# Performance work log

Measured on AMD Instinct MI355X. Metric: run time of the kernel, lower is better.

Reference implementation:

```python
import jax, jax.numpy as jnp
import numpy as np

C = 512
C8 = C // 8
B, H, W = 4, 64, 64


def _conv1x1(x, w, b):
    # x: (B, Cin, H, W), w: (Cout, Cin), b: (Cout,)
    return jnp.einsum('oi,bihw->bohw', w, x) + b[None, :, None, None]


def setup_inputs() -> dict:
    key = jax.random.key(0)
    ks = jax.random.split(key, 16)
    s = 0.02
    inp = {
        'x': jax.random.normal(ks[0], (B, C, H, W), dtype=jnp.float32),
        'wpq': jax.random.normal(ks[1], (C8, C), dtype=jnp.float32) * s,
        'bpq': jnp.zeros((C8,), jnp.float32),
        'wpk': jax.random.normal(ks[2], (C8, C), dtype=jnp.float32) * s,
        'bpk': jnp.zeros((C8,), jnp.float32),
        'wpv': jax.random.normal(ks[3], (C, C), dtype=jnp.float32) * s,
        'bpv': jnp.zeros((C,), jnp.float32),
        'wcq': jax.random.normal(ks[4], (C, C), dtype=jnp.float32) * s,
        'bcq': jnp.zeros((C,), jnp.float32),
        'wck': jax.random.normal(ks[5], (C, C), dtype=jnp.float32) * s,
        'bck': jnp.zeros((C,), jnp.float32),
        'wcv': jax.random.normal(ks[6], (C, C), dtype=jnp.float32) * s,
        'bcv': jnp.zeros((C,), jnp.float32),
        # gammas are zero-init in torch; use small nonzero values so both
        # attention branches contribute to the output numerically.
        'gpos': jax.random.normal(ks[7], (1,), dtype=jnp.float32) * 0.1,
        'gchan': jax.random.normal(ks[8], (1,), dtype=jnp.float32) * 0.1,
    }
    return inp


def reference(x, wpq, bpq, wpk, bpk, wpv, bpv, wcq, bcq, wck, bck, wcv, bcv, gpos, gchan):
    b, c, h, w = x.shape
    n = h * w
    # ---- position attention ----
    pos_q = _conv1x1(x, wpq, bpq).reshape(b, C8, n)           # (b, C/8, N)
    pos_k = _conv1x1(x, wpk, bpk).reshape(b, C8, n)           # (b, C/8, N)
    pos_v = _conv1x1(x, wpv, bpv).reshape(b, c, n)            # (b, C, N)
    pos_attn = jax.nn.softmax(jnp.einsum('bcq,bck->bqk', pos_q, pos_k), axis=-1)  # (b, N, N)
    pos_out = jnp.einsum('bck,bqk->bcq', pos_v, pos_attn).reshape(b, c, h, w)
    pos_out = gpos * pos_out + x
    # ---- channel attention ----
    chan_q = _conv1x1(pos_out, wcq, bcq).reshape(b, c, n)
    chan_k = _conv1x1(pos_out, wck, bck).reshape(b, c, n)
    chan_v = _conv1x1(pos_out, wcv, bcv).reshape(b, c, n)
    chan_attn = jax.nn.softmax(jnp.einsum('bin,bjn->bij', chan_q, chan_k), axis=-1)  # (b, C, C)
    chan_out = jnp.einsum('bij,bjn->bin', chan_attn, chan_v).reshape(b, c, h, w)
    return gchan * chan_out + pos_out
```

## Files before the change

kernel.cpp:

```cpp
#include <hip/hip_runtime.h>
#include <hip/hip_bf16.h>
#include <math.h>

typedef __bf16 bf16;
typedef __attribute__((ext_vector_type(8))) __bf16 bf16x8;
typedef __attribute__((ext_vector_type(4))) __bf16 bf16x4;
typedef __attribute__((ext_vector_type(4))) float f32x4;

#define DEVI static __device__ __forceinline__

DEVI int swzb(int row, int ch) { return ((ch ^ (row & 7)) << 4); }

DEVI void gl_lds16(const void* g, void* l) {
  __builtin_amdgcn_global_load_lds(
      (const __attribute__((address_space(1))) unsigned int*)g,
      (__attribute__((address_space(3))) unsigned int*)l, 16, 0, 0);
}

template<int N> DEVI void wait_vm() {
  if constexpr (N == 0) asm volatile("s_waitcnt vmcnt(0)" ::: "memory");
  else if constexpr (N == 4) asm volatile("s_waitcnt vmcnt(4)" ::: "memory");
  else if constexpr (N == 6) asm volatile("s_waitcnt vmcnt(6)" ::: "memory");
  else if constexpr (N == 8) asm volatile("s_waitcnt vmcnt(8)" ::: "memory");
}
DEVI void sbar() {
  __builtin_amdgcn_sched_barrier(0);
  __builtin_amdgcn_s_barrier();
  __builtin_amdgcn_sched_barrier(0);
}

__global__ __launch_bounds__(256) void prep_weights(
    const float* __restrict__ wpq, const float* __restrict__ wpk,
    const float* __restrict__ wpv, const float* __restrict__ wcq,
    const float* __restrict__ wck, const float* __restrict__ wcv,
    const float* __restrict__ bpq, const float* __restrict__ bpk,
    bf16* __restrict__ wqk, bf16* __restrict__ wpvb, bf16* __restrict__ wcqb,
    bf16* __restrict__ wckb, bf16* __restrict__ wcvT, float* __restrict__ bqk)
{
  int i = blockIdx.x * 256 + threadIdx.x;
  switch (blockIdx.y) {
    case 0: if (i < 64*512)  wqk[i]          = (bf16)wpq[i]; break;
    case 1: if (i < 64*512)  wqk[64*512 + i] = (bf16)wpk[i]; break;
    case 2: if (i < 512*512) wpvb[i] = (bf16)wpv[i]; break;
    case 3: if (i < 512*512) wcqb[i] = (bf16)wcq[i]; break;
    case 4: if (i < 512*512) wckb[i] = (bf16)wck[i]; break;
    case 5: if (i < 512*512) { int t = i >> 9, j = i & 511; wcvT[i] = (bf16)wcv[j*512 + t]; } break;
    case 6: if (i < 64) bqk[i] = bpq[i]; else if (i < 128) bqk[i] = bpk[i - 64]; break;
  }
}

__global__ __launch_bounds__(256) void transpose_x(const float* __restrict__ x, bf16* __restrict__ xbT)
{
  __shared__ float t[32][33];
  int b = blockIdx.z, n0 = blockIdx.x * 32, c0 = blockIdx.y * 32;
  int tx = threadIdx.x & 31, ty = threadIdx.x >> 5;
#pragma unroll
  for (int i = 0; i < 4; ++i)
    t[ty + 8*i][tx] = x[((size_t)b*512 + c0 + ty + 8*i)*4096 + n0 + tx];
  __syncthreads();
#pragma unroll
  for (int i = 0; i < 4; ++i)
    xbT[((size_t)b*4096 + n0 + ty + 8*i)*512 + c0 + tx] = (bf16)t[tx][ty + 8*i];
}

struct GemmP {
  const bf16* A; const bf16* Bt; void* C;
  long aS, bS;
  long cSbytes;
  int lda, ldb, ldc, K;
  const float* biasM; const float* biasN;
  const float* e_bq; const float* e_v; const float* e_u; const float* e_bk; float e_nn;
  long vS, uS;
  const float* gchan; const float* Abv; const bf16* Pres; long abvS, presS;
};

template<int BM, int BN, int BIAS, int EPI>
__global__ __launch_bounds__(256) void gemm_k(GemmP p)
{
  constexpr int QF = BM / 32;
  constexpr int CF = BN / 32;
  constexpr int NBUF = (BM + BN <= 192) ? 3 : 2;
  constexpr int LOADS = (BM + BN) / 32;
  __shared__ __align__(16) char sa[NBUF][BM * 128];
  __shared__ __align__(16) char sb[NBUF][BN * 128];
  const int tid = threadIdx.x, lane = tid & 63, w = tid >> 6;
  const int g = lane >> 4, l15 = lane & 15;
  const int bm = blockIdx.x * BM, bn = blockIdx.y * BN, bz = blockIdx.z;
  const bf16* A  = p.A  + (size_t)bz * p.aS;
  const bf16* Bt = p.Bt + (size_t)bz * p.bS;
  char* Cb = (char*)p.C + (size_t)bz * p.cSbytes;
  const int wm = (w & 1) * (BM / 2), wn = (w >> 1) * (BN / 2);
  const int srow = tid >> 3, sch = tid & 7;

  f32x4 acc[QF][CF];
#pragma unroll
  for (int i = 0; i < QF; ++i)
#pragma unroll
    for (int j = 0; j < CF; ++j) acc[i][j] = f32x4{0.f, 0.f, 0.f, 0.f};

  auto stage = [&](int k0, int bi) {
#pragma unroll
    for (int it = 0; it < BM / 32; ++it) {
      int r = it * 32 + srow;
      gl_lds16(A + (size_t)(bm + r) * p.lda + k0 + ((sch ^ (r & 7)) * 8),
               sa[bi] + (it * 32 + w * 8) * 128);
    }
#pragma unroll
    for (int it = 0; it < BN / 32; ++it) {
      int r = it * 32 + srow;
      gl_lds16(Bt + (size_t)(bn + r) * p.ldb + k0 + ((sch ^ (r & 7)) * 8),
               sb[bi] + (it * 32 + w * 8) * 128);
    }
  };
  auto compute = [&](int bi) {
#pragma unroll
    for (int kc = 0; kc < 2; ++kc) {
      bf16x8 af[QF], bfr[CF];
#pragma unroll
      for (int qf = 0; qf < QF; ++qf) {
        int row = wm + 16 * qf + l15;
        af[qf] = *(const bf16x8*)(sa[bi] + row * 128 + swzb(row, g + 4 * kc));
      }
#pragma unroll
      for (int cf = 0; cf < CF; ++cf) {
        int row = wn + 16 * cf + l15;
        bfr[cf] = *(const bf16x8*)(sb[bi] + row * 128 + swzb(row, g + 4 * kc));
      }
      __builtin_amdgcn_s_setprio(1);
#pragma unroll
      for (int qf = 0; qf < QF; ++qf)
#pragma unroll
        for (int cf = 0; cf < CF; ++cf)
          acc[qf][cf] = __builtin_amdgcn_mfma_f32_16x16x32_bf16(af[qf], bfr[cf], acc[qf][cf], 0, 0, 0);
      __builtin_amdgcn_s_setprio(0);
    }
  };

  const int nk = p.K >> 6;
  if constexpr (NBUF == 3) {
    stage(0, 0);
    if (nk > 1) { stage(64, 1); wait_vm<LOADS>(); } else wait_vm<0>();
    sbar();
    int bi = 0;
    for (int t = 0; t < nk; ++t) {
      int b2 = bi + 2; if (b2 >= 3) b2 -= 3;
      if (t + 2 < nk) stage((t + 2) << 6, b2);
      compute(bi);
      if (t + 1 < nk) {
        if (t + 2 < nk) wait_vm<LOADS>(); else wait_vm<0>();
        sbar();
      }
      if (++bi == 3) bi = 0;
    }
  } else {
    stage(0, 0);
    __syncthreads();
    for (int t = 0; t < nk; ++t) {
      const int cur = t & 1;
      if (t + 1 < nk) stage((t + 1) << 6, cur ^ 1);
      compute(cur);
      __syncthreads();
    }
  }

  float gc = 0.f;
  const float* AbvB = nullptr; const bf16* PresB = nullptr;
  const float* eV = nullptr; const float* eU = nullptr;
  if (EPI == 3) { gc = p.gchan[0]; AbvB = p.Abv + (size_t)bz * p.abvS; PresB = p.Pres + (size_t)bz * p.presS; }
  if (EPI == 2) { eV = p.e_v + (size_t)bz * p.vS; eU = p.e_u + (size_t)bz * p.uS; }

#pragma unroll
  for (int qf = 0; qf < QF; ++qf)
#pragma unroll
    for (int cf = 0; cf < CF; ++cf)
#pragma unroll
      for (int r = 0; r < 4; ++r) {
        int m = bm + wm + 16 * qf + 4 * g + r;
        int n = bn + wn + 16 * cf + l15;
        float v = acc[qf][cf][r];
        if (BIAS == 1) v += p.biasM[m];
        if (BIAS == 2) v += p.biasN[n];
        size_t idx = (size_t)m * p.ldc + n;
        if (EPI == 0) ((bf16*)Cb)[idx] = (bf16)v;
        else if (EPI == 1) ((float*)Cb)[idx] = v;
        else if (EPI == 2) {
          v += p.e_bq[m] * eV[n] + eU[m] * p.e_bk[n] + p.e_nn * p.e_bq[m] * p.e_bk[n];
          ((float*)Cb)[idx] = v;
        } else {
          v = gc * (v + AbvB[m]) + (float)PresB[idx];
          ((float*)Cb)[idx] = v;
        }
      }
}

__global__ __launch_bounds__(512, 4) void flash_pos(
    const bf16* __restrict__ QKT, const bf16* __restrict__ Vv,
    const float* __restrict__ x, const float* __restrict__ gpos,
    bf16* __restrict__ Pb, bf16* __restrict__ PTb)
{
  extern __shared__ char sm[];
  char* Vlds = sm + 16384;
  char* Plds = sm + 49152;
  float* Och  = (float*)sm;
  float* lsum = (float*)(sm + 57344);

  const int tid = threadIdx.x, lane = tid & 63, w = tid >> 6;
  const int g = lane >> 4, l15 = lane & 15;
  const int wq = w & 3;
  const int wh = w >> 2;
  const int phys = blockIdx.x;
  const int b  = (phys & 7) >> 1;
  const int ch = phys & 1;
  const int q0 = (phys >> 3) << 6;
  const int c0 = ch << 8;

  const bf16* QKTb = QKT + (size_t)b * 4096 * 128;
  const bf16* Vb   = Vv  + (size_t)b * 512 * 4096;

  const bf16* qrow = QKTb + (size_t)(q0 + 16 * wq + l15) * 128;
  bf16x8 qa0 = *(const bf16x8*)(qrow + 8 * g);
  bf16x8 qa1 = *(const bf16x8*)(qrow + 32 + 8 * g);

  f32x4 acc[4][2];
#pragma unroll
  for (int i = 0; i < 4; ++i) { acc[i][0] = f32x4{0.f,0.f,0.f,0.f}; acc[i][1] = f32x4{0.f,0.f,0.f,0.f}; }
  f32x4 l_r = f32x4{0.f, 0.f, 0.f, 0.f};

  const int srow = tid >> 3, sch = tid & 7;
  const bf16* Ksrc = QKTb + (size_t)srow * 128 + 64 + ((sch ^ (srow & 7)) * 8);

  gl_lds16(Ksrc, sm + w * 1024);
#pragma unroll
  for (int it = 0; it < 4; ++it) {
    int r = it * 64 + srow;
    gl_lds16(Vb + (size_t)(c0 + r) * 4096 + ((sch ^ (r & 7)) * 8),
             Vlds + (it * 64 + w * 8) * 128);
  }
  asm volatile("s_waitcnt vmcnt(0)" ::: "memory");
  sbar();

  for (int t = 0; t < 64; ++t) {
    const char* Kcur = sm + ((t & 1) << 13);
    char* Knext = sm + (((t + 1) & 1) << 13);
    const int ktn = (t + 1) & 63;
    gl_lds16(Ksrc + (size_t)ktn * 8192, Knext + w * 1024);
    __builtin_amdgcn_sched_barrier(0);
    f32x4 s0 = f32x4{0.f,0.f,0.f,0.f}, s1 = f32x4{0.f,0.f,0.f,0.f};
    {
      const int r0 = 32 * wh + l15, r1 = r0 + 16;
      bf16x8 k00 = *(const bf16x8*)(Kcur + r0 * 128 + swzb(r0, g));
      bf16x8 k01 = *(const bf16x8*)(Kcur + r0 * 128 + swzb(r0, g + 4));
      bf16x8 k10 = *(const bf16x8*)(Kcur + r1 * 128 + swzb(r1, g));
      bf16x8 k11 = *(const bf16x8*)(Kcur + r1 * 128 + swzb(r1, g + 4));
      __builtin_amdgcn_s_setprio(1);
      s0 = __builtin_amdgcn_mfma_f32_16x16x32_bf16(qa0, k00, s0, 0, 0, 0);
      s0 = __builtin_amdgcn_mfma_f32_16x16x32_bf16(qa1, k01, s0, 0, 0, 0);
      s1 = __builtin_amdgcn_mfma_f32_16x16x32_bf16(qa0, k10, s1, 0, 0, 0);
      s1 = __builtin_amdgcn_mfma_f32_16x16x32_bf16(qa1, k11, s1, 0, 0, 0);
      __builtin_amdgcn_s_setprio(0);
    }
#pragma unroll
    for (int r = 0; r < 4; ++r) {
      float e0 = __expf(s0[r]), e1 = __expf(s1[r]);
      l_r[r] += e0 + e1;
      int row = 16 * wq + 4 * g + r;
      int ca = 32 * wh + l15, cb = ca + 16;
      *(bf16*)(Plds + row * 128 + (((ca >> 3) ^ (row & 7)) << 4) + ((ca & 7) * 2)) = (bf16)e0;
      *(bf16*)(Plds + row * 128 + (((cb >> 3) ^ (row & 7)) << 4) + ((cb & 7) * 2)) = (bf16)e1;
    }
    asm volatile("s_waitcnt vmcnt(1) lgkmcnt(0)" ::: "memory");
    sbar();
    __builtin_amdgcn_s_setprio(1);
#pragma unroll
    for (int kc = 0; kc < 2; ++kc) {
      const int vra = 32 * w + l15, vrb = vra + 16;
      bf16x8 v0 = *(const bf16x8*)(Vlds + vra * 128 + swzb(vra, g + 4 * kc));
      bf16x8 v1 = *(const bf16x8*)(Vlds + vrb * 128 + swzb(vrb, g + 4 * kc));
#pragma unroll
      for (int qf = 0; qf < 4; ++qf) {
        int row = 16 * qf + l15;
        bf16x8 ap = *(const bf16x8*)(Plds + row * 128 + swzb(row, g + 4 * kc));
        acc[qf][0] = __builtin_amdgcn_mfma_f32_16x16x32_bf16(ap, v0, acc[qf][0], 0, 0, 0);
        acc[qf][1] = __builtin_amdgcn_mfma_f32_16x16x32_bf16(ap, v1, acc[qf][1], 0, 0, 0);
      }
    }
    __builtin_amdgcn_s_setprio(0);
    asm volatile("s_waitcnt vmcnt(0) lgkmcnt(0)" ::: "memory");
    sbar();
#pragma unroll
    for (int it = 0; it < 4; ++it) {
      int r = it * 64 + srow;
      gl_lds16(Vb + (size_t)(c0 + r) * 4096 + ktn * 64 + ((sch ^ (r & 7)) * 8),
               Vlds + (it * 64 + w * 8) * 128);
    }
  }
  asm volatile("s_waitcnt vmcnt(0) lgkmcnt(0)" ::: "memory");
  sbar();

#pragma unroll
  for (int off = 1; off < 16; off <<= 1) {
#pragma unroll
    for (int r = 0; r < 4; ++r) l_r[r] += __shfl_xor(l_r[r], off);
  }
  if (l15 == 0)
#pragma unroll
    for (int r = 0; r < 4; ++r) lsum[wh * 64 + 16 * wq + 4 * g + r] = l_r[r];
  __syncthreads();

  const float gp = gpos[0];
  for (int j = 0; j < 2; ++j) {
    if ((w >> 2) == j) {
#pragma unroll
      for (int qf = 0; qf < 4; ++qf) {
        float inv[4];
#pragma unroll
        for (int r = 0; r < 4; ++r) {
          int qi = 16 * qf + 4 * g + r;
          inv[r] = gp / (lsum[qi] + lsum[64 + qi]);
        }
#pragma unroll
        for (int cf = 0; cf < 2; ++cf) {
          int cl = 32 * (w & 3) + 16 * cf + l15;
#pragma unroll
          for (int r = 0; r < 4; ++r)
            Och[cl * 68 + 16 * qf + 4 * g + r] = acc[qf][cf][r] * inv[r];
        }
      }
    }
    __syncthreads();
    {
      int cl = tid >> 2, qs = (tid & 3) * 16;
      int cg = c0 + 128 * j + cl;
      const float* xr = x + ((size_t)b * 512 + cg) * 4096 + q0 + qs;
      float* och = Och + cl * 68 + qs;
      float tmp[16];
#pragma unroll
      for (int i = 0; i < 16; ++i) { tmp[i] = och[i] + xr[i]; och[i] = tmp[i]; }
      bf16x8 o0, o1;
#pragma unroll
      for (int i = 0; i < 8; ++i) { o0[i] = (bf16)tmp[i]; o1[i] = (bf16)tmp[i + 8]; }
      bf16* pr = Pb + ((size_t)b * 512 + cg) * 4096 + q0 + qs;
      *(bf16x8*)pr = o0; *(bf16x8*)(pr + 8) = o1;
    }
    __syncthreads();
    {
      int q = tid >> 3, cs = (tid & 7) * 16;
      float tmp[16];
#pragma unroll
      for (int i = 0; i < 16; ++i) tmp[i] = Och[(cs + i) * 68 + q];
      bf16x8 o0, o1;
#pragma unroll
      for (int i = 0; i < 8; ++i) { o0[i] = (bf16)tmp[i]; o1[i] = (bf16)tmp[i + 8]; }
      bf16* pt = PTb + ((size_t)b * 4096 + q0 + q) * 512 + c0 + 128 * j + cs;
      *(bf16x8*)pt = o0; *(bf16x8*)(pt + 8) = o1;
    }
    __syncthreads();
  }
}

__global__ __launch_bounds__(256) void row_sum(const bf16* __restrict__ Pb, float* __restrict__ r)
{
  int wid = blockIdx.x * 4 + (threadIdx.x >> 6);
  int lane = threadIdx.x & 63;
  const bf16* row = Pb + (size_t)wid * 4096;
  float s = 0.f;
#pragma unroll
  for (int i = 0; i < 8; ++i) {
    bf16x8 v = ((const bf16x8*)row)[lane + 64 * i];
#pragma unroll
    for (int j = 0; j < 8; ++j) s += (float)v[j];
  }
#pragma unroll
  for (int off = 1; off < 64; off <<= 1) s += __shfl_xor(s, off);
  if (lane == 0) r[wid] = s;
}

__global__ __launch_bounds__(256) void uv_kernel(
    const float* __restrict__ wcq, const float* __restrict__ wck,
    const float* __restrict__ r, float* __restrict__ u, float* __restrict__ v)
{
  int b = blockIdx.z;
  int i = blockIdx.x * 256 + threadIdx.x;
  const float* rb = r + b * 512;
  const float* wrow = (blockIdx.y ? wck : wcq) + (size_t)i * 512;
  float s = 0.f;
  for (int t = 0; t < 512; ++t) s += wrow[t] * rb[t];
  (blockIdx.y ? v : u)[b * 512 + i] = s;
}

__global__ __launch_bounds__(256) void softmax_chan(
    const float* __restrict__ L, const float* __restrict__ bcv,
    bf16* __restrict__ Ab, float* __restrict__ Abv)
{
  int b = blockIdx.z;
  int i = blockIdx.x * 4 + (threadIdx.x >> 6);
  int lane = threadIdx.x & 63;
  const float* row = L + ((size_t)b * 512 + i) * 512;
  f32x4 v0 = ((const f32x4*)row)[lane];
  f32x4 v1 = ((const f32x4*)row)[lane + 64];
  float mx = fmaxf(fmaxf(fmaxf(v0[0], v0[1]), fmaxf(v0[2], v0[3])),
                   fmaxf(fmaxf(v1[0], v1[1]), fmaxf(v1[2], v1[3])));
#pragma unroll
  for (int off = 1; off < 64; off <<= 1) mx = fmaxf(mx, __shfl_xor(mx, off));
  float e[8]; float s = 0.f;
#pragma unroll
  for (int k = 0; k < 4; ++k) { e[k] = __expf(v0[k] - mx); s += e[k]; }
#pragma unroll
  for (int k = 0; k < 4; ++k) { e[4 + k] = __expf(v1[k] - mx); s += e[4 + k]; }
#pragma unroll
  for (int off = 1; off < 64; off <<= 1) s += __shfl_xor(s, off);
  float inv = 1.f / s;
  bf16x4 a0, a1;
  const f32x4 bv0 = ((const f32x4*)bcv)[lane];
  const f32x4 bv1 = ((const f32x4*)bcv)[lane + 64];
  float pb = 0.f;
#pragma unroll
  for (int k = 0; k < 4; ++k) {
    float p0 = e[k] * inv, p1 = e[4 + k] * inv;
    a0[k] = (bf16)p0; a1[k] = (bf16)p1;
    pb += p0 * bv0[k] + p1 * bv1[k];
  }
  bf16* arow = Ab + ((size_t)b * 512 + i) * 512;
  *(bf16x4*)(arow + 4 * lane) = a0;
  *(bf16x4*)(arow + 256 + 4 * lane) = a1;
#pragma unroll
  for (int off = 1; off < 64; off <<= 1) pb += __shfl_xor(pb, off);
  if (lane == 0) Abv[b * 512 + i] = pb;
}

extern "C" void kernel_launch(void* const* d_in, const int* in_sizes, int n_in,
                              void* d_out, int out_size, void* d_ws, size_t ws_size,
                              hipStream_t stream)
{
  const float* x    = (const float*)d_in[0];
  const float* wpq  = (const float*)d_in[1];
  const float* bpq  = (const float*)d_in[2];
  const float* wpk  = (const float*)d_in[3];
  const float* bpk  = (const float*)d_in[4];
  const float* wpv  = (const float*)d_in[5];
  const float* bpv  = (const float*)d_in[6];
  const float* wcq  = (const float*)d_in[7];
  const float* bcq  = (const float*)d_in[8];
  const float* wck  = (const float*)d_in[9];
  const float* bck  = (const float*)d_in[10];
  const float* wcv  = (const float*)d_in[11];
  const float* bcv  = (const float*)d_in[12];
  const float* gpos = (const float*)d_in[13];
  const float* gch  = (const float*)d_in[14];
  float* out = (float*)d_out;

  char* ws = (char*)d_ws;
  size_t off = 0;
  auto alloc = [&](size_t bytes) -> char* {
    char* p = ws + off; off = (off + bytes + 255) & ~(size_t)255; return p;
  };
  bf16*  xbT  = (bf16*)alloc(4UL * 4096 * 512 * 2);
  bf16*  QKT  = (bf16*)alloc(4UL * 4096 * 128 * 2);
  bf16*  V    = (bf16*)alloc(4UL * 512 * 4096 * 2);
  bf16*  Pb   = (bf16*)alloc(4UL * 512 * 4096 * 2);
  bf16*  PTb  = (bf16*)alloc(4UL * 4096 * 512 * 2);
  bf16*  G    = (bf16*)alloc(4UL * 512 * 512 * 2);
  bf16*  M1   = (bf16*)alloc(4UL * 512 * 512 * 2);
  float* Lws  = (float*)alloc(4UL * 512 * 512 * 4);
  bf16*  Ab   = (bf16*)alloc(4UL * 512 * 512 * 2);
  bf16*  B2   = (bf16*)alloc(4UL * 512 * 512 * 2);
  bf16*  wqk  = (bf16*)alloc(128UL * 512 * 2);
  bf16*  wpvb = (bf16*)alloc(512UL * 512 * 2);
  bf16*  wcqb = (bf16*)alloc(512UL * 512 * 2);
  bf16*  wckb = (bf16*)alloc(512UL * 512 * 2);
  bf16*  wcvT = (bf16*)alloc(512UL * 512 * 2);
  float* bqk  = (float*)alloc(128 * 4);
  float* rws  = (float*)alloc(4UL * 512 * 4);
  float* uws  = (float*)alloc(4UL * 512 * 4);
  float* vws  = (float*)alloc(4UL * 512 * 4);
  float* Abv  = (float*)alloc(4UL * 512 * 4);
  if (off > ws_size) return;

  prep_weights<<<dim3(1024, 7, 1), 256, 0, stream>>>(wpq, wpk, wpv, wcq, wck, wcv,
                                                     bpq, bpk, wqk, wpvb, wcqb, wckb, wcvT, bqk);
  transpose_x<<<dim3(128, 16, 4), 256, 0, stream>>>(x, xbT);

  GemmP p{};
  p = GemmP{};
  p.A = xbT; p.aS = 4096L * 512; p.lda = 512;
  p.Bt = wqk; p.bS = 0; p.ldb = 512;
  p.C = QKT; p.cSbytes = 4096L * 128 * 2; p.ldc = 128;
  p.K = 512; p.biasN = bqk;
  gemm_k<128, 64, 2, 0><<<dim3(32, 2, 4), 256, 0, stream>>>(p);

  p = GemmP{};
  p.A = wpvb; p.aS = 0; p.lda = 512;
  p.Bt = xbT; p.bS = 4096L * 512; p.ldb = 512;
  p.C = V; p.cSbytes = 512L * 4096 * 2; p.ldc = 4096;
  p.K = 512; p.biasM = bpv;
  gemm_k<128, 128, 1, 0><<<dim3(4, 32, 4), 256, 0, stream>>>(p);

  flash_pos<<<dim3(512, 1, 1), 512, 57856, stream>>>(QKT, V, x, gpos, Pb, PTb);

  p = GemmP{};
  p.A = Pb; p.aS = 512L * 4096; p.lda = 4096;
  p.Bt = Pb; p.bS = 512L * 4096; p.ldb = 4096;
  p.C = G; p.cSbytes = 512L * 512 * 2; p.ldc = 512;
  p.K = 4096;
  gemm_k<64, 64, 0, 0><<<dim3(8, 8, 4), 256, 0, stream>>>(p);

  row_sum<<<dim3(512, 1, 1), 256, 0, stream>>>(Pb, rws);
  uv_kernel<<<dim3(2, 2, 4), 256, 0, stream>>>(wcq, wck, rws, uws, vws);

  p = GemmP{};
  p.A = wcqb; p.aS = 0; p.lda = 512;
  p.Bt = G; p.bS = 512L * 512; p.ldb = 512;
  p.C = M1; p.cSbytes = 512L * 512 * 2; p.ldc = 512;
  p.K = 512;
  gemm_k<64, 64, 0, 0><<<dim3(8, 8, 4), 256, 0, stream>>>(p);

  p = GemmP{};
  p.A = M1; p.aS = 512L * 512; p.lda = 512;
  p.Bt = wckb; p.bS = 0; p.ldb = 512;
  p.C = Lws; p.cSbytes = 512L * 512 * 4; p.ldc = 512;
  p.K = 512;
  p.e_bq = bcq; p.e_v = vws; p.vS = 512; p.e_u = uws; p.uS = 512; p.e_bk = bck; p.e_nn = 4096.f;
  gemm_k<64, 64, 0, 2><<<dim3(8, 8, 4), 256, 0, stream>>>(p);

  softmax_chan<<<dim3(128, 1, 4), 256, 0, stream>>>(Lws, bcv, Ab, Abv);

  p = GemmP{};
  p.A = Ab; p.aS = 512L * 512; p.lda = 512;
  p.Bt = wcvT; p.bS = 0; p.ldb = 512;
  p.C = B2; p.cSbytes = 512L * 512 * 2; p.ldc = 512;
  p.K = 512;
  gemm_k<64, 64, 0, 0><<<dim3(8, 8, 4), 256, 0, stream>>>(p);

  p = GemmP{};
  p.A = B2; p.aS = 512L * 512; p.lda = 512;
  p.Bt = PTb; p.bS = 4096L * 512; p.ldb = 512;
  p.C = out; p.cSbytes = 512L * 4096 * 4; p.ldc = 4096;
  p.K = 512;
  p.gchan = gch; p.Abv = Abv; p.abvS = 512; p.Pres = Pb; p.presS = 512L * 4096;
  gemm_k<128, 128, 0, 3><<<dim3(4, 32, 4), 256, 0, stream>>>(p);
}
```

Baseline: 269.6 us.

## Process all 512 channels per flash_pos block to avoid duplicate QK/softmax work

Each flash_pos block now covers all 512 value channels for its 64 queries instead of splitting channels across two blocks. This halves the grid and removes the duplicated QK^T scores and exp computation that both channel halves previously repeated. In exchange each wave holds twice the accumulators, the V tile in LDS doubles (about 90KB of shared memory), and occupancy drops to 2 blocks per CU. The query-to-block mapping is also remapped.

```diff
diff --git a/kernel.cpp b/kernel.cpp
--- a/kernel.cpp
+++ b/kernel.cpp
@@ -193,16 +193,16 @@
       }
 }
 
-__global__ __launch_bounds__(512, 4) void flash_pos(
+__global__ __launch_bounds__(512, 2) void flash_pos(
     const bf16* __restrict__ QKT, const bf16* __restrict__ Vv,
     const float* __restrict__ x, const float* __restrict__ gpos,
     bf16* __restrict__ Pb, bf16* __restrict__ PTb)
 {
   extern __shared__ char sm[];
   char* Vlds = sm + 16384;
-  char* Plds = sm + 49152;
+  char* Plds = sm + 81920;
   float* Och  = (float*)sm;
-  float* lsum = (float*)(sm + 57344);
+  float* lsum = (float*)(sm + 90112);
 
   const int tid = threadIdx.x, lane = tid & 63, w = tid >> 6;
   const int g = lane >> 4, l15 = lane & 15;
@@ -210,9 +210,7 @@
   const int wh = w >> 2;
   const int phys = blockIdx.x;
   const int b  = (phys & 7) >> 1;
-  const int ch = phys & 1;
-  const int q0 = (phys >> 3) << 6;
-  const int c0 = ch << 8;
+  const int q0 = ((((phys & 1) << 5) | (phys >> 3))) << 6;
 
   const bf16* QKTb = QKT + (size_t)b * 4096 * 128;
   const bf16* Vb   = Vv  + (size_t)b * 512 * 4096;
@@ -221,9 +219,11 @@
   bf16x8 qa0 = *(const bf16x8*)(qrow + 8 * g);
   bf16x8 qa1 = *(const bf16x8*)(qrow + 32 + 8 * g);
 
-  f32x4 acc[4][2];
-#pragma unroll
-  for (int i = 0; i < 4; ++i) { acc[i][0] = f32x4{0.f,0.f,0.f,0.f}; acc[i][1] = f32x4{0.f,0.f,0.f,0.f}; }
+  f32x4 acc[4][4];
+#pragma unroll
+  for (int i = 0; i < 4; ++i)
+#pragma unroll
+    for (int j = 0; j < 4; ++j) acc[i][j] = f32x4{0.f,0.f,0.f,0.f};
   f32x4 l_r = f32x4{0.f, 0.f, 0.f, 0.f};
 
   const int srow = tid >> 3, sch = tid & 7;
@@ -231,9 +231,9 @@
 
   gl_lds16(Ksrc, sm + w * 1024);
 #pragma unroll
-  for (int it = 0; it < 4; ++it) {
+  for (int it = 0; it < 8; ++it) {
     int r = it * 64 + srow;
-    gl_lds16(Vb + (size_t)(c0 + r) * 4096 + ((sch ^ (r & 7)) * 8),
+    gl_lds16(Vb + (size_t)r * 4096 + ((sch ^ (r & 7)) * 8),
              Vlds + (it * 64 + w * 8) * 128);
   }
   asm volatile("s_waitcnt vmcnt(0)" ::: "memory");
@@ -273,24 +273,28 @@
     __builtin_amdgcn_s_setprio(1);
 #pragma unroll
     for (int kc = 0; kc < 2; ++kc) {
-      const int vra = 32 * w + l15, vrb = vra + 16;
-      bf16x8 v0 = *(const bf16x8*)(Vlds + vra * 128 + swzb(vra, g + 4 * kc));
-      bf16x8 v1 = *(const bf16x8*)(Vlds + vrb * 128 + swzb(vrb, g + 4 * kc));
+      bf16x8 vf[4];
+#pragma unroll
+      for (int cf = 0; cf < 4; ++cf) {
+        int vr = 64 * w + 16 * cf + l15;
+        vf[cf] = *(const bf16x8*)(Vlds + vr * 128 + swzb(vr, g + 4 * kc));
+      }
 #pragma unroll
       for (int qf = 0; qf < 4; ++qf) {
         int row = 16 * qf + l15;
         bf16x8 ap = *(const bf16x8*)(Plds + row * 128 + swzb(row, g + 4 * kc));
-        acc[qf][0] = __builtin_amdgcn_mfma_f32_16x16x32_bf16(ap, v0, acc[qf][0], 0, 0, 0);
-        acc[qf][1] = __builtin_amdgcn_mfma_f32_16x16x32_bf16(ap, v1, acc[qf][1], 0, 0, 0);
+#pragma unroll
+        for (int cf = 0; cf < 4; ++cf)
+          acc[qf][cf] = __builtin_amdgcn_mfma_f32_16x16x32_bf16(ap, vf[cf], acc[qf][cf], 0, 0, 0);
       }
     }
     __builtin_amdgcn_s_setprio(0);
     asm volatile("s_waitcnt vmcnt(0) lgkmcnt(0)" ::: "memory");
     sbar();
 #pragma unroll
-    for (int it = 0; it < 4; ++it) {
+    for (int it = 0; it < 8; ++it) {
       int r = it * 64 + srow;
-      gl_lds16(Vb + (size_t)(c0 + r) * 4096 + ktn * 64 + ((sch ^ (r & 7)) * 8),
+      gl_lds16(Vb + (size_t)r * 4096 + ktn * 64 + ((sch ^ (r & 7)) * 8),
                Vlds + (it * 64 + w * 8) * 128);
     }
   }
@@ -308,8 +312,8 @@
   __syncthreads();
 
   const float gp = gpos[0];
-  for (int j = 0; j < 2; ++j) {
-    if ((w >> 2) == j) {
+  for (int j = 0; j < 4; ++j) {
+    if ((w >> 1) == j) {
 #pragma unroll
       for (int qf = 0; qf < 4; ++qf) {
         float inv[4];
@@ -319,8 +323,8 @@
           inv[r] = gp / (lsum[qi] + lsum[64 + qi]);
         }
 #pragma unroll
-        for (int cf = 0; cf < 2; ++cf) {
-          int cl = 32 * (w & 3) + 16 * cf + l15;
+        for (int cf = 0; cf < 4; ++cf) {
+          int cl = 64 * (w & 1) + 16 * cf + l15;
 #pragma unroll
           for (int r = 0; r < 4; ++r)
             Och[cl * 68 + 16 * qf + 4 * g + r] = acc[qf][cf][r] * inv[r];
@@ -330,7 +334,7 @@
     __syncthreads();
     {
       int cl = tid >> 2, qs = (tid & 3) * 16;
-      int cg = c0 + 128 * j + cl;
+      int cg = 128 * j + cl;
       const float* xr = x + ((size_t)b * 512 + cg) * 4096 + q0 + qs;
       float* och = Och + cl * 68 + qs;
       float tmp[16];
@@ -351,7 +355,7 @@
       bf16x8 o0, o1;
 #pragma unroll
       for (int i = 0; i < 8; ++i) { o0[i] = (bf16)tmp[i]; o1[i] = (bf16)tmp[i + 8]; }
-      bf16* pt = PTb + ((size_t)b * 4096 + q0 + q) * 512 + c0 + 128 * j + cs;
+      bf16* pt = PTb + ((size_t)b * 4096 + q0 + q) * 512 + 128 * j + cs;
       *(bf16x8*)pt = o0; *(bf16x8*)(pt + 8) = o1;
     }
     __syncthreads();
@@ -495,7 +499,9 @@
   p.K = 512; p.biasM = bpv;
   gemm_k<128, 128, 1, 0><<<dim3(4, 32, 4), 256, 0, stream>>>(p);
 
-  flash_pos<<<dim3(512, 1, 1), 512, 57856, stream>>>(QKT, V, x, gpos, Pb, PTb);
+  (void)hipFuncSetAttribute((const void*)flash_pos,
+                            hipFuncAttributeMaxDynamicSharedMemorySize, 90624);
+  flash_pos<<<dim3(256, 1, 1), 512, 90624, stream>>>(QKT, V, x, gpos, Pb, PTb);
 
   p = GemmP{};
   p.A = Pb; p.aS = 512L * 4096; p.lda = 4096;
```

Result: slower. 281.4 us (+4.4%).

## Fuse row sums into flash_pos via atomics and remap GEMM block order

Applied to the files above, without the earlier changes.

Removes the separate row_sum kernel. flash_pos now accumulates per-channel row sums of the residual output in fp32 with atomicAdd, into a buffer zeroed by a memset. Separately, the V projection and final output GEMMs launch as a 1D grid whose block-to-tile mapping mirrors flash_pos's XCD/batch interleave, aiming for better L2 locality across chiplets. The atomics add contention and a memset launch, and the row sum is now taken in fp32 before bf16 rounding, which changes numerics slightly.

```diff
diff --git a/kernel.cpp b/kernel.cpp
--- a/kernel.cpp
+++ b/kernel.cpp
@@ -68,6 +68,7 @@
   long aS, bS;
   long cSbytes;
   int lda, ldb, ldc, K;
+  int remap;
   const float* biasM; const float* biasN;
   const float* e_bq; const float* e_v; const float* e_u; const float* e_bk; float e_nn;
   long vS, uS;
@@ -85,7 +86,14 @@
   __shared__ __align__(16) char sb[NBUF][BN * 128];
   const int tid = threadIdx.x, lane = tid & 63, w = tid >> 6;
   const int g = lane >> 4, l15 = lane & 15;
-  const int bm = blockIdx.x * BM, bn = blockIdx.y * BN, bz = blockIdx.z;
+  int bx = blockIdx.x, by = blockIdx.y, bz = blockIdx.z;
+  if (p.remap) {
+    int ph = blockIdx.x;
+    bz = (ph & 7) >> 1;
+    int idx = ((ph & 1) << 6) | (ph >> 3);
+    bx = idx & 3; by = idx >> 2;
+  }
+  const int bm = bx * BM, bn = by * BN;
   const bf16* A  = p.A  + (size_t)bz * p.aS;
   const bf16* Bt = p.Bt + (size_t)bz * p.bS;
   char* Cb = (char*)p.C + (size_t)bz * p.cSbytes;
@@ -196,7 +204,7 @@
 __global__ __launch_bounds__(512, 4) void flash_pos(
     const bf16* __restrict__ QKT, const bf16* __restrict__ Vv,
     const float* __restrict__ x, const float* __restrict__ gpos,
-    bf16* __restrict__ Pb, bf16* __restrict__ PTb)
+    bf16* __restrict__ Pb, bf16* __restrict__ PTb, float* __restrict__ rws)
 {
   extern __shared__ char sm[];
   char* Vlds = sm + 16384;
@@ -334,13 +342,15 @@
       const float* xr = x + ((size_t)b * 512 + cg) * 4096 + q0 + qs;
       float* och = Och + cl * 68 + qs;
       float tmp[16];
-#pragma unroll
-      for (int i = 0; i < 16; ++i) { tmp[i] = och[i] + xr[i]; och[i] = tmp[i]; }
+      float s16 = 0.f;
+#pragma unroll
+      for (int i = 0; i < 16; ++i) { tmp[i] = och[i] + xr[i]; och[i] = tmp[i]; s16 += tmp[i]; }
       bf16x8 o0, o1;
 #pragma unroll
       for (int i = 0; i < 8; ++i) { o0[i] = (bf16)tmp[i]; o1[i] = (bf16)tmp[i + 8]; }
       bf16* pr = Pb + ((size_t)b * 512 + cg) * 4096 + q0 + qs;
       *(bf16x8*)pr = o0; *(bf16x8*)(pr + 8) = o1;
+      atomicAdd(rws + b * 512 + cg, s16);
     }
     __syncthreads();
     {
@@ -356,23 +366,6 @@
     }
     __syncthreads();
   }
-}
-
-__global__ __launch_bounds__(256) void row_sum(const bf16* __restrict__ Pb, float* __restrict__ r)
-{
-  int wid = blockIdx.x * 4 + (threadIdx.x >> 6);
-  int lane = threadIdx.x & 63;
-  const bf16* row = Pb + (size_t)wid * 4096;
-  float s = 0.f;
-#pragma unroll
-  for (int i = 0; i < 8; ++i) {
-    bf16x8 v = ((const bf16x8*)row)[lane + 64 * i];
-#pragma unroll
-    for (int j = 0; j < 8; ++j) s += (float)v[j];
-  }
-#pragma unroll
-  for (int off = 1; off < 64; off <<= 1) s += __shfl_xor(s, off);
-  if (lane == 0) r[wid] = s;
 }
 
 __global__ __launch_bounds__(256) void uv_kernel(
@@ -479,6 +472,7 @@
   prep_weights<<<dim3(1024, 7, 1), 256, 0, stream>>>(wpq, wpk, wpv, wcq, wck, wcv,
                                                      bpq, bpk, wqk, wpvb, wcqb, wckb, wcvT, bqk);
   transpose_x<<<dim3(128, 16, 4), 256, 0, stream>>>(x, xbT);
+  (void)hipMemsetAsync(rws, 0, 4UL * 512 * 4, stream);
 
   GemmP p{};
   p = GemmP{};
@@ -492,10 +486,10 @@
   p.A = wpvb; p.aS = 0; p.lda = 512;
   p.Bt = xbT; p.bS = 4096L * 512; p.ldb = 512;
   p.C = V; p.cSbytes = 512L * 4096 * 2; p.ldc = 4096;
-  p.K = 512; p.biasM = bpv;
-  gemm_k<128, 128, 1, 0><<<dim3(4, 32, 4), 256, 0, stream>>>(p);
-
-  flash_pos<<<dim3(512, 1, 1), 512, 57856, stream>>>(QKT, V, x, gpos, Pb, PTb);
+  p.K = 512; p.biasM = bpv; p.remap = 1;
+  gemm_k<128, 128, 1, 0><<<dim3(512, 1, 1), 256, 0, stream>>>(p);
+
+  flash_pos<<<dim3(512, 1, 1), 512, 57856, stream>>>(QKT, V, x, gpos, Pb, PTb, rws);
 
   p = GemmP{};
   p.A = Pb; p.aS = 512L * 4096; p.lda = 4096;
@@ -504,7 +498,6 @@
   p.K = 4096;
   gemm_k<64, 64, 0, 0><<<dim3(8, 8, 4), 256, 0, stream>>>(p);
 
-  row_sum<<<dim3(512, 1, 1), 256, 0, stream>>>(Pb, rws);
   uv_kernel<<<dim3(2, 2, 4), 256, 0, stream>>>(wcq, wck, rws, uws, vws);
 
   p = GemmP{};
@@ -537,5 +530,6 @@
   p.C = out; p.cSbytes = 512L * 4096 * 4; p.ldc = 4096;
   p.K = 512;
   p.gchan = gch; p.Abv = Abv; p.abvS = 512; p.Pres = Pb; p.presS = 512L * 4096;
-  gemm_k<128, 128, 0, 3><<<dim3(4, 32, 4), 256, 0, stream>>>(p);
-}
+  p.remap = 1;
+  gemm_k<128, 128, 0, 3><<<dim3(512, 1, 1), 256, 0, stream>>>(p);
+}
```

Result: slower. 410.3 us (+52.2%).
